# Performance work log

Measured on AMD Instinct MI355X. Metric: run time of the kernel, lower is better.

## Reference

```python
import jax, jax.numpy as jnp
import numpy as np

T, B, D_IN, D_LAT, D_OUT = 512, 256, 256, 512, 256

def setup_inputs() -> dict:
    key = jax.random.key(0)
    k = jax.random.split(key, 4)
    scale_h = 1.0 / np.sqrt(D_IN + D_LAT)
    scale_o = 1.0 / np.sqrt(D_LAT)
    return {
        "x": jax.random.normal(k[0], (T, B, D_IN), dtype=jnp.float32),
        "h": jnp.zeros((B, D_LAT), dtype=jnp.float32),
        "Wh": jax.random.normal(k[1], (D_IN + D_LAT, D_LAT), dtype=jnp.float32) * scale_h,
        "bh": jnp.zeros((D_LAT,), dtype=jnp.float32),
        "Wo": jax.random.normal(k[2], (D_LAT, D_OUT), dtype=jnp.float32) * scale_o,
        "bo": jnp.zeros((D_OUT,), dtype=jnp.float32),
    }

def reference(x, h, Wh, bh, Wo, bo):
    # Split Wh into input / hidden blocks: cat(x,h) @ Wh == x@Wx + h@Wr
    Wx = Wh[:D_IN]    # [D_IN, D_LAT]
    Wr = Wh[D_IN:]    # [D_LAT, D_LAT]

    def step(h_prev, x_t):
        h_next = jax.nn.relu(x_t @ Wx + h_prev @ Wr + bh)  # [B, D_LAT]
        return h_next, h_next

    _, hidden_states = jax.lax.scan(step, h, x)            # [T, B, D_LAT]
    outputs = hidden_states @ Wo + bo                      # [T, B, D_OUT]
    return outputs, hidden_states
```

## Files before the change

### kernel.cpp

```cpp
#include <hip/hip_runtime.h>
#include <hip/hip_bf16.h>


#define TT 512
#define BB 256
#define DIN 256
#define DLAT 512
#define DOUT 256

typedef short bf16x8 __attribute__((ext_vector_type(8)));
typedef int   i32x4  __attribute__((ext_vector_type(4)));
typedef float f32x4  __attribute__((ext_vector_type(4)));

__device__ __forceinline__ unsigned short f2bf(float f) {
  union { float f; unsigned u; } v; v.f = f;
  unsigned r = v.u + (((v.u >> 16) & 1u) + 0x7fffu);
  return (unsigned short)(r >> 16);
}
__device__ __forceinline__ unsigned pack2(float a, float b) {
  return (unsigned)f2bf(a) | ((unsigned)f2bf(b) << 16);
}

__device__ __forceinline__ i32x4 load_b128_sc(const void* p) {
  i32x4 r;
  asm volatile("global_load_dwordx4 %0, %1, off sc0 sc1" : "=v"(r) : "v"(p) : "memory");
  return r;
}
__device__ __forceinline__ void store_short_sc(void* p, unsigned v) {
  asm volatile("global_store_short %0, %1, off sc0 sc1" :: "v"(p), "v"(v) : "memory");
}
__device__ __forceinline__ void store_flag_sc(void* p, int v) {
  asm volatile("global_store_dword %0, %1, off sc0 sc1" :: "v"(p), "v"(v) : "memory");
}
__device__ __forceinline__ int load_flag_sc(const void* p) {
  int r;
  asm volatile("global_load_dword %0, %1, off sc0 sc1\n\ts_waitcnt vmcnt(0)"
               : "=v"(r) : "v"(p) : "memory");
  return r;
}
__device__ __forceinline__ void waitvm0() {
  asm volatile("s_waitcnt vmcnt(0)" ::: "memory");
  __builtin_amdgcn_sched_barrier(0);
}
__device__ __forceinline__ void waitvm8() {
  asm volatile("s_waitcnt vmcnt(8)" ::: "memory");
  __builtin_amdgcn_sched_barrier(0);
}

__global__ __launch_bounds__(256) void prep_kernel(
    const float* __restrict__ Wh, const float* __restrict__ Wo,
    unsigned short* __restrict__ wx, unsigned short* __restrict__ wr,
    unsigned short* __restrict__ wo) {
  int id = blockIdx.x * 256 + threadIdx.x;
  {
    int k = id >> 9, col = id & 511;
    int s = col >> 7, c = col & 127;
    wr[(s << 16) + (((c << 9) | k) ^ ((c & 7) << 3))] = f2bf(Wh[(256 + k) * 512 + col]);
  }
  if (id < 131072) {
    int k = id >> 9, col = id & 511;
    int s = col >> 7, c = col & 127;
    wx[(s << 15) + (((c << 8) | k) ^ ((c & 7) << 3))] = f2bf(Wh[id]);
  }
  if (id < 131072) {
    int k = id >> 8, col = id & 255;
    int s = col >> 7, c = col & 127;
    wo[(s << 16) + (((c << 9) | k) ^ ((c & 7) << 3))] = f2bf(Wo[id]);
  }
}

template <int K, int NSTR, int SLBITS>
__global__ __launch_bounds__(256) void gemm_bias(
    const float* __restrict__ Xg, const unsigned short* __restrict__ Wp,
    const float* __restrict__ bias, float* __restrict__ Cg) {
  __shared__ unsigned short ldsW[128 * K];
  __shared__ unsigned short ldsA[128 * 64];
  const int tid = threadIdx.x;
  const int s = blockIdx.x & ((1 << SLBITS) - 1);
  const size_t r0 = (size_t)(blockIdx.x >> SLBITS) * 128;
  {
    const uint4* src = (const uint4*)(Wp + (size_t)s * 128 * K);
    uint4* dst = (uint4*)ldsW;
#pragma unroll
    for (int i = 0; i < (128 * K / 8) / 256; ++i) dst[tid + 256 * i] = src[tid + 256 * i];
  }
  const int lane = tid & 63, wid = tid >> 6;
  const int wm = wid >> 1, wn = wid & 1;
  const int cl = lane & 15, kh = lane >> 4;
  f32x4 acc[4][4];
#pragma unroll
  for (int nf = 0; nf < 4; ++nf) {
    float bv = bias[s * 128 + wn * 64 + nf * 16 + cl];
#pragma unroll
    for (int mf = 0; mf < 4; ++mf) { f32x4 t = {bv, bv, bv, bv}; acc[mf][nf] = t; }
  }
  __syncthreads();
  for (int k0 = 0; k0 < K; k0 += 64) {
#pragma unroll
    for (int i = 0; i < 8; ++i) {
      int g = tid + 256 * i;
      int row = g >> 4, kg = g & 15;
      const float4 v = *(const float4*)&Xg[(r0 + row) * K + (k0 + kg * 4)];
      int idx = (row * 64 + kg * 4) ^ ((row & 7) << 3);
      uint2 u; u.x = pack2(v.x, v.y); u.y = pack2(v.z, v.w);
      *(uint2*)&ldsA[idx] = u;
    }
    __syncthreads();
#pragma unroll
    for (int kk = 0; kk < 2; ++kk) {
      bf16x8 aF[4], bF[4];
#pragma unroll
      for (int mf = 0; mf < 4; ++mf) {
        int row = wm * 64 + mf * 16 + cl;
        int kl = kk * 32 + 8 * kh;
        aF[mf] = *(const bf16x8*)&ldsA[(row * 64 + kl) ^ ((row & 7) << 3)];
      }
#pragma unroll
      for (int nf = 0; nf < 4; ++nf) {
        int cc = wn * 64 + nf * 16 + cl;
        int k = k0 + kk * 32 + 8 * kh;
        bF[nf] = *(const bf16x8*)&ldsW[(cc * K + k) ^ ((cc & 7) << 3)];
      }
#pragma unroll
      for (int mf = 0; mf < 4; ++mf)
#pragma unroll
        for (int nf = 0; nf < 4; ++nf)
          acc[mf][nf] = __builtin_amdgcn_mfma_f32_16x16x32_bf16(aF[mf], bF[nf], acc[mf][nf], 0, 0, 0);
    }
    __syncthreads();
  }
#pragma unroll
  for (int mf = 0; mf < 4; ++mf)
#pragma unroll
    for (int nf = 0; nf < 4; ++nf)
#pragma unroll
      for (int j = 0; j < 4; ++j)
        Cg[(r0 + wm * 64 + mf * 16 + kh * 4 + j) * NSTR + s * 128 + wn * 64 + nf * 16 + cl] =
            acc[mf][nf][j];
}

__global__ __launch_bounds__(256) void scan_kernel(
    const float* __restrict__ h0, const unsigned short* __restrict__ WrP,
    float* __restrict__ Hid, int* __restrict__ flags, unsigned short* __restrict__ ex) {
  const int tid = threadIdx.x, lane = tid & 63, wid = tid >> 6;
  const int g = blockIdx.x & 15, c = blockIdx.x >> 4;
  const int r0 = g * 16;
  const int c0 = c * 128;
  const int cl = lane & 15, kh = lane >> 4;
  const int wc = c0 + wid * 32;
  int* flags4 = flags + g * 4;

  bf16x8 bw0[16], bw1[16];
  {
    const unsigned short* base = WrP + (size_t)c * 65536;
    const int cb0 = wid * 32 + cl, cb1 = cb0 + 16;
#pragma unroll
    for (int kk = 0; kk < 16; ++kk) {
      int k = kk * 32 + 8 * kh;
      bw0[kk] = *(const bf16x8*)(base + (((cb0 << 9) | k) ^ ((cb0 & 7) << 3)));
      bw1[kk] = *(const bf16x8*)(base + (((cb1 << 9) | k) ^ ((cb1 & 7) << 3)));
    }
  }

  {
    int row = tid >> 4;
    int cb = (tid & 15) * 8;
    unsigned short* exW = ex + (16 + g) * 8192 + row * 512 + c0 + cb;
    const float* hs = h0 + (size_t)(r0 + row) * DLAT + c0 + cb;
#pragma unroll
    for (int q = 0; q < 8; ++q) store_short_sc(exW + q, f2bf(hs[q]));
    waitvm0();
  }
  __syncthreads();
  if (tid == 0) store_flag_sc(&flags4[c], 0);

  for (int t = 0; t < TT; ++t) {
    float ai0[4], ai1[4];
    const float* At = Hid + (size_t)t * (BB * DLAT);
#pragma unroll
    for (int j = 0; j < 4; ++j) {
      ai0[j] = At[(r0 + kh * 4 + j) * DLAT + wc + cl];
      ai1[j] = At[(r0 + kh * 4 + j) * DLAT + wc + 16 + cl];
    }
    if (tid < 4) {
      while (load_flag_sc(&flags4[tid]) < t) {}
    }
    __syncthreads();

    const unsigned short* exR = ex + (((t + 1) & 1) * 16 + g) * 8192;
    i32x4 fa[16];
#pragma unroll
    for (int kk = 0; kk < 16; ++kk)
      fa[kk] = load_b128_sc(exR + cl * 512 + kk * 32 + kh * 8);

    f32x4 acc0 = {ai0[0], ai0[1], ai0[2], ai0[3]};
    f32x4 acc1 = {ai1[0], ai1[1], ai1[2], ai1[3]};
    waitvm8();
#pragma unroll
    for (int kk = 0; kk < 8; ++kk) {
      bf16x8 aF = __builtin_bit_cast(bf16x8, fa[kk]);
      acc0 = __builtin_amdgcn_mfma_f32_16x16x32_bf16(aF, bw0[kk], acc0, 0, 0, 0);
      acc1 = __builtin_amdgcn_mfma_f32_16x16x32_bf16(aF, bw1[kk], acc1, 0, 0, 0);
    }
    waitvm0();
#pragma unroll
    for (int kk = 8; kk < 16; ++kk) {
      bf16x8 aF = __builtin_bit_cast(bf16x8, fa[kk]);
      acc0 = __builtin_amdgcn_mfma_f32_16x16x32_bf16(aF, bw0[kk], acc0, 0, 0, 0);
      acc1 = __builtin_amdgcn_mfma_f32_16x16x32_bf16(aF, bw1[kk], acc1, 0, 0, 0);
    }

    float* Ht = Hid + (size_t)t * (BB * DLAT);
    unsigned short* exW = ex + ((t & 1) * 16 + g) * 8192;
    float v0[4], v1[4];
#pragma unroll
    for (int j = 0; j < 4; ++j) {
      v0[j] = fmaxf(acc0[j], 0.f);
      v1[j] = fmaxf(acc1[j], 0.f);
      Ht[(r0 + kh * 4 + j) * DLAT + wc + cl] = v0[j];
      Ht[(r0 + kh * 4 + j) * DLAT + wc + 16 + cl] = v1[j];
    }
    if (t < TT - 1) {
#pragma unroll
      for (int j = 0; j < 4; ++j) {
        store_short_sc(exW + (kh * 4 + j) * 512 + wc + cl, f2bf(v0[j]));
        store_short_sc(exW + (kh * 4 + j) * 512 + wc + 16 + cl, f2bf(v1[j]));
      }
      waitvm0();
      __syncthreads();
      if (tid == 0) store_flag_sc(&flags4[c], t + 1);
    }
  }
}

extern "C" void kernel_launch(void* const* d_in, const int* in_sizes, int n_in,
                              void* d_out, int out_size, void* d_ws, size_t ws_size,
                              hipStream_t stream) {
  const float* x  = (const float*)d_in[0];
  const float* h0 = (const float*)d_in[1];
  const float* Wh = (const float*)d_in[2];
  const float* bh = (const float*)d_in[3];
  const float* Wo = (const float*)d_in[4];
  const float* bo = (const float*)d_in[5];
  float* Out = (float*)d_out;
  float* Hid = Out + (size_t)TT * BB * DOUT;

  unsigned short* ws_wx = (unsigned short*)d_ws;
  unsigned short* ws_wr = ws_wx + 131072;
  unsigned short* ws_wo = ws_wr + 262144;
  int* flags = (int*)(ws_wo + 131072);
  unsigned short* ex = (unsigned short*)(flags + 64);

  hipMemsetAsync(flags, 0xFF, 64 * sizeof(int), stream);
  prep_kernel<<<1024, 256, 0, stream>>>(Wh, Wo, ws_wx, ws_wr, ws_wo);
  gemm_bias<256, 512, 2><<<4096, 256, 0, stream>>>(x, ws_wx, bh, Hid);
  scan_kernel<<<64, 256, 0, stream>>>(h0, ws_wr, Hid, flags, ex);
  gemm_bias<512, 256, 1><<<2048, 256, 0, stream>>>(Hid, ws_wo, bo, Out);
}
```

Baseline: 2.479 ms.

## Keep own hidden slice in LDS and coalesce cross-block exchange stores

Each block now stores its own bf16 hidden-state slice in shared memory and reorders its K loop so its own four K chunks are consumed first from LDS. Only the other twelve chunks are loaded from the global exchange buffer after the flag wait, which shortens the critical path. The exchange writes become one 128-bit store per thread, staged through LDS, instead of eight scattered short stores. The fp32 Hid stores are moved after the flag publish so they are off the dependency chain, at the cost of an extra __syncthreads per step.

```diff
diff --git a/kernel.cpp b/kernel.cpp
--- a/kernel.cpp
+++ b/kernel.cpp
@@ -26,8 +26,8 @@
   asm volatile("global_load_dwordx4 %0, %1, off sc0 sc1" : "=v"(r) : "v"(p) : "memory");
   return r;
 }
-__device__ __forceinline__ void store_short_sc(void* p, unsigned v) {
-  asm volatile("global_store_short %0, %1, off sc0 sc1" :: "v"(p), "v"(v) : "memory");
+__device__ __forceinline__ void store_b128_sc(void* p, i32x4 v) {
+  asm volatile("global_store_dwordx4 %0, %1, off sc0 sc1" :: "v"(p), "v"(v) : "memory");
 }
 __device__ __forceinline__ void store_flag_sc(void* p, int v) {
   asm volatile("global_store_dword %0, %1, off sc0 sc1" :: "v"(p), "v"(v) : "memory");
@@ -42,8 +42,8 @@
   asm volatile("s_waitcnt vmcnt(0)" ::: "memory");
   __builtin_amdgcn_sched_barrier(0);
 }
-__device__ __forceinline__ void waitvm8() {
-  asm volatile("s_waitcnt vmcnt(8)" ::: "memory");
+__device__ __forceinline__ void waitvm6() {
+  asm volatile("s_waitcnt vmcnt(6)" ::: "memory");
   __builtin_amdgcn_sched_barrier(0);
 }
 
@@ -142,6 +142,7 @@
 __global__ __launch_bounds__(256) void scan_kernel(
     const float* __restrict__ h0, const unsigned short* __restrict__ WrP,
     float* __restrict__ Hid, int* __restrict__ flags, unsigned short* __restrict__ ex) {
+  __shared__ unsigned short lt[16][136];
   const int tid = threadIdx.x, lane = tid & 63, wid = tid >> 6;
   const int g = blockIdx.x & 15, c = blockIdx.x >> 4;
   const int r0 = g * 16;
@@ -150,25 +151,29 @@
   const int wc = c0 + wid * 32;
   int* flags4 = flags + g * 4;
 
-  bf16x8 bw0[16], bw1[16];
+  bf16x8 bwR0[16], bwR1[16];
   {
     const unsigned short* base = WrP + (size_t)c * 65536;
     const int cb0 = wid * 32 + cl, cb1 = cb0 + 16;
 #pragma unroll
-    for (int kk = 0; kk < 16; ++kk) {
+    for (int i = 0; i < 16; ++i) {
+      int kk = (c * 4 + i) & 15;
       int k = kk * 32 + 8 * kh;
-      bw0[kk] = *(const bf16x8*)(base + (((cb0 << 9) | k) ^ ((cb0 & 7) << 3)));
-      bw1[kk] = *(const bf16x8*)(base + (((cb1 << 9) | k) ^ ((cb1 & 7) << 3)));
-    }
-  }
-
-  {
-    int row = tid >> 4;
-    int cb = (tid & 15) * 8;
-    unsigned short* exW = ex + (16 + g) * 8192 + row * 512 + c0 + cb;
-    const float* hs = h0 + (size_t)(r0 + row) * DLAT + c0 + cb;
-#pragma unroll
-    for (int q = 0; q < 8; ++q) store_short_sc(exW + q, f2bf(hs[q]));
+      bwR0[i] = *(const bf16x8*)(base + (((cb0 << 9) | k) ^ ((cb0 & 7) << 3)));
+      bwR1[i] = *(const bf16x8*)(base + (((cb1 << 9) | k) ^ ((cb1 & 7) << 3)));
+    }
+  }
+
+  {
+    int r = tid >> 4, cb = (tid & 15) * 8;
+    const float* hs = h0 + (size_t)(r0 + r) * DLAT + c0 + cb;
+    float4 a = *(const float4*)&hs[0];
+    float4 b = *(const float4*)&hs[4];
+    i32x4 w;
+    w[0] = (int)pack2(a.x, a.y); w[1] = (int)pack2(a.z, a.w);
+    w[2] = (int)pack2(b.x, b.y); w[3] = (int)pack2(b.z, b.w);
+    *(i32x4*)&lt[r][cb] = w;
+    store_b128_sc(ex + (size_t)(16 + g) * 8192 + r * 512 + c0 + cb, w);
     waitvm0();
   }
   __syncthreads();
@@ -182,53 +187,68 @@
       ai0[j] = At[(r0 + kh * 4 + j) * DLAT + wc + cl];
       ai1[j] = At[(r0 + kh * 4 + j) * DLAT + wc + 16 + cl];
     }
+    i32x4 of[4];
+#pragma unroll
+    for (int i = 0; i < 4; ++i) of[i] = *(const i32x4*)&lt[cl][i * 32 + kh * 8];
     if (tid < 4) {
       while (load_flag_sc(&flags4[tid]) < t) {}
     }
     __syncthreads();
 
-    const unsigned short* exR = ex + (((t + 1) & 1) * 16 + g) * 8192;
-    i32x4 fa[16];
-#pragma unroll
-    for (int kk = 0; kk < 16; ++kk)
-      fa[kk] = load_b128_sc(exR + cl * 512 + kk * 32 + kh * 8);
-
     f32x4 acc0 = {ai0[0], ai0[1], ai0[2], ai0[3]};
     f32x4 acc1 = {ai1[0], ai1[1], ai1[2], ai1[3]};
-    waitvm8();
-#pragma unroll
-    for (int kk = 0; kk < 8; ++kk) {
-      bf16x8 aF = __builtin_bit_cast(bf16x8, fa[kk]);
-      acc0 = __builtin_amdgcn_mfma_f32_16x16x32_bf16(aF, bw0[kk], acc0, 0, 0, 0);
-      acc1 = __builtin_amdgcn_mfma_f32_16x16x32_bf16(aF, bw1[kk], acc1, 0, 0, 0);
+    __builtin_amdgcn_sched_barrier(0);
+
+    const unsigned short* exR = ex + (size_t)(((t + 1) & 1) * 16 + g) * 8192;
+    i32x4 fa[12];
+#pragma unroll
+    for (int i = 0; i < 12; ++i) {
+      int kk = (c * 4 + 4 + i) & 15;
+      fa[i] = load_b128_sc(exR + cl * 512 + kk * 32 + kh * 8);
+    }
+#pragma unroll
+    for (int i = 0; i < 4; ++i) {
+      bf16x8 aF = __builtin_bit_cast(bf16x8, of[i]);
+      acc0 = __builtin_amdgcn_mfma_f32_16x16x32_bf16(aF, bwR0[i], acc0, 0, 0, 0);
+      acc1 = __builtin_amdgcn_mfma_f32_16x16x32_bf16(aF, bwR1[i], acc1, 0, 0, 0);
+    }
+    waitvm6();
+#pragma unroll
+    for (int i = 0; i < 6; ++i) {
+      bf16x8 aF = __builtin_bit_cast(bf16x8, fa[i]);
+      acc0 = __builtin_amdgcn_mfma_f32_16x16x32_bf16(aF, bwR0[4 + i], acc0, 0, 0, 0);
+      acc1 = __builtin_amdgcn_mfma_f32_16x16x32_bf16(aF, bwR1[4 + i], acc1, 0, 0, 0);
     }
     waitvm0();
 #pragma unroll
-    for (int kk = 8; kk < 16; ++kk) {
-      bf16x8 aF = __builtin_bit_cast(bf16x8, fa[kk]);
-      acc0 = __builtin_amdgcn_mfma_f32_16x16x32_bf16(aF, bw0[kk], acc0, 0, 0, 0);
-      acc1 = __builtin_amdgcn_mfma_f32_16x16x32_bf16(aF, bw1[kk], acc1, 0, 0, 0);
-    }
-
-    float* Ht = Hid + (size_t)t * (BB * DLAT);
-    unsigned short* exW = ex + ((t & 1) * 16 + g) * 8192;
+    for (int i = 6; i < 12; ++i) {
+      bf16x8 aF = __builtin_bit_cast(bf16x8, fa[i]);
+      acc0 = __builtin_amdgcn_mfma_f32_16x16x32_bf16(aF, bwR0[4 + i], acc0, 0, 0, 0);
+      acc1 = __builtin_amdgcn_mfma_f32_16x16x32_bf16(aF, bwR1[4 + i], acc1, 0, 0, 0);
+    }
+
     float v0[4], v1[4];
 #pragma unroll
     for (int j = 0; j < 4; ++j) {
       v0[j] = fmaxf(acc0[j], 0.f);
       v1[j] = fmaxf(acc1[j], 0.f);
-      Ht[(r0 + kh * 4 + j) * DLAT + wc + cl] = v0[j];
-      Ht[(r0 + kh * 4 + j) * DLAT + wc + 16 + cl] = v1[j];
+      lt[kh * 4 + j][wid * 32 + cl] = f2bf(v0[j]);
+      lt[kh * 4 + j][wid * 32 + 16 + cl] = f2bf(v1[j]);
     }
     if (t < TT - 1) {
-#pragma unroll
-      for (int j = 0; j < 4; ++j) {
-        store_short_sc(exW + (kh * 4 + j) * 512 + wc + cl, f2bf(v0[j]));
-        store_short_sc(exW + (kh * 4 + j) * 512 + wc + 16 + cl, f2bf(v1[j]));
-      }
+      __syncthreads();
+      int r = tid >> 4, cb = (tid & 15) * 8;
+      i32x4 w = *(const i32x4*)&lt[r][cb];
+      store_b128_sc(ex + (size_t)((t & 1) * 16 + g) * 8192 + r * 512 + c0 + cb, w);
       waitvm0();
       __syncthreads();
       if (tid == 0) store_flag_sc(&flags4[c], t + 1);
+    }
+    float* Ht = Hid + (size_t)t * (BB * DLAT);
+#pragma unroll
+    for (int j = 0; j < 4; ++j) {
+      Ht[(r0 + kh * 4 + j) * DLAT + wc + cl] = v0[j];
+      Ht[(r0 + kh * 4 + j) * DLAT + wc + 16 + cl] = v1[j];
     }
   }
 }
```

Measured after the change: 2.285 ms. 1.08x faster.
